# Kernel optimization log

Hardware: AMD Instinct MI355X
Metric: run time of the kernel (lower is better)

Reference implementation:

```python
import jax, jax.numpy as jnp
import numpy as np

D_MODEL = 1024
NUM_HEADS = 16
D_K = D_MODEL // NUM_HEADS


def setup_inputs() -> dict:
    key = jax.random.key(0)
    ks = jax.random.split(key, 12)
    B, S = 4, 2048
    scale = 1.0 / np.sqrt(D_MODEL)
    inp = {
        "query": jax.random.normal(ks[0], (B, S, D_MODEL), dtype=jnp.float32),
        "key": jax.random.normal(ks[1], (B, S, D_MODEL), dtype=jnp.float32),
        "value": jax.random.normal(ks[2], (B, S, D_MODEL), dtype=jnp.float32),
        "Wq": jax.random.normal(ks[3], (D_MODEL, D_MODEL), dtype=jnp.float32) * scale,
        "bq": jnp.zeros((D_MODEL,), dtype=jnp.float32),
        "Wk": jax.random.normal(ks[4], (D_MODEL, D_MODEL), dtype=jnp.float32) * scale,
        "bk": jnp.zeros((D_MODEL,), dtype=jnp.float32),
        "Wv": jax.random.normal(ks[5], (D_MODEL, D_MODEL), dtype=jnp.float32) * scale,
        "bv": jnp.zeros((D_MODEL,), dtype=jnp.float32),
        "Wo": jax.random.normal(ks[6], (D_MODEL, D_MODEL), dtype=jnp.float32) * scale,
        "bo": jnp.zeros((D_MODEL,), dtype=jnp.float32),
    }
    return inp


def reference(query, key, value, Wq, bq, Wk, bk, Wv, bv, Wo, bo):
    B, S, _ = query.shape
    # project and split heads: [B, S, D] -> [B, H, S, d_k]
    def split_heads(x):
        return x.reshape(B, -1, NUM_HEADS, D_K).transpose(0, 2, 1, 3)

    q = split_heads(query @ Wq + bq)
    k = split_heads(key @ Wk + bk)
    v = split_heads(value @ Wv + bv)

    # scores: [B, H, Sq, Sk]
    scores = jnp.einsum("bhqd,bhkd->bhqk", q, k) / jnp.sqrt(jnp.float32(D_K))
    p_attn = jax.nn.softmax(scores, axis=-1)
    out = jnp.einsum("bhqk,bhkd->bhqd", p_attn, v)  # [B, H, Sq, d_k]

    out = out.transpose(0, 2, 1, 3).reshape(B, -1, NUM_HEADS * D_K)
    return out @ Wo + bo
```

## Files before the change

kernel.cpp:

```cpp
#include <hip/hip_runtime.h>
#include <hip/hip_bf16.h>

#define D_MODEL 1024
#define SEQ     2048
#define BATCH   4
#define HEADS   16
#define DKK     64
#define MTOT    (BATCH*SEQ)

typedef __attribute__((ext_vector_type(8)))  __bf16 bf16x8;
typedef __attribute__((ext_vector_type(4)))  float  f32x4;
typedef __attribute__((ext_vector_type(16))) float  f32x16;
typedef unsigned short u16;
typedef __attribute__((address_space(1))) const unsigned GU;
typedef __attribute__((address_space(3))) unsigned LU;

__device__ __forceinline__ u16 f2bf(float f) {
    unsigned u = __builtin_bit_cast(unsigned, f);
    u += 0x7FFFu + ((u >> 16) & 1u);
    return (u16)(u >> 16);
}

__device__ __forceinline__ unsigned pk2(float a, float b) {
    u16 x = __builtin_bit_cast(u16, (__bf16)a);
    u16 y = __builtin_bit_cast(u16, (__bf16)b);
    return (unsigned)x | ((unsigned)y << 16);
}

__device__ __forceinline__ float exp2_hw(float x) {
    return __builtin_amdgcn_exp2f(x);
}

__global__ void f2b3_kernel(const float* __restrict__ q, const float* __restrict__ k,
                            const float* __restrict__ v,
                            u16* __restrict__ oq, u16* __restrict__ ok, u16* __restrict__ ov,
                            int n4) {
    const float* in = (blockIdx.y == 0) ? q : (blockIdx.y == 1) ? k : v;
    u16* out = (blockIdx.y == 0) ? oq : (blockIdx.y == 1) ? ok : ov;
    int stride = gridDim.x * blockDim.x;
    for (int i = blockIdx.x * blockDim.x + threadIdx.x; i < n4; i += stride) {
        float4 x = reinterpret_cast<const float4*>(in)[i];
        ushort4 o;
        o.x = f2bf(x.x); o.y = f2bf(x.y); o.z = f2bf(x.z); o.w = f2bf(x.w);
        reinterpret_cast<ushort4*>(out)[i] = o;
    }
}

__global__ void wtrans4_kernel(const float* __restrict__ W0, const float* __restrict__ W1,
                               const float* __restrict__ W2, const float* __restrict__ W3,
                               u16* __restrict__ T0, u16* __restrict__ T1,
                               u16* __restrict__ T2, u16* __restrict__ T3) {
    const float* W = (blockIdx.z == 0) ? W0 : (blockIdx.z == 1) ? W1 : (blockIdx.z == 2) ? W2 : W3;
    u16* Wt = (blockIdx.z == 0) ? T0 : (blockIdx.z == 1) ? T1 : (blockIdx.z == 2) ? T2 : T3;
    __shared__ float t[32][33];
    int bx = blockIdx.x * 32, by = blockIdx.y * 32;
    int x = threadIdx.x, y0 = threadIdx.y;
    for (int y = y0; y < 32; y += 8)
        t[y][x] = W[(size_t)(by + y) * D_MODEL + bx + x];
    __syncthreads();
    for (int y = y0; y < 32; y += 8)
        Wt[(size_t)(bx + y) * D_MODEL + by + x] = f2bf(t[x][y]);
}

__global__ __launch_bounds__(256) void gemm_pipe(
        const u16* __restrict__ A0, const u16* __restrict__ A1, const u16* __restrict__ A2,
        const u16* __restrict__ B0, const u16* __restrict__ B1, const u16* __restrict__ B2,
        const float* __restrict__ bi0, const float* __restrict__ bi1, const float* __restrict__ bi2,
        u16* __restrict__ o0, u16* __restrict__ o1, u16* __restrict__ o2,
        float* __restrict__ outf, int mode, float scale0)
{
    __shared__ __align__(16) char smem[3][16384];

    const int lin = blockIdx.x;
    const int xcd = lin & 7, slot = lin >> 3;
    const int cpx = gridDim.x >> 3;
    const int work = xcd * cpx + slot;
    const int xb = work & 7;
    const int yz = work >> 3;
    const int z = yz >> 6, yb = yz & 63;
    const int m0 = yb * 128, n0 = xb * 128;

    const u16* A  = (z == 0) ? A0 : (z == 1) ? A1 : A2;
    const u16* Bt = (z == 0) ? B0 : (z == 1) ? B1 : B2;
    const float* bias = (z == 0) ? bi0 : (z == 1) ? bi1 : bi2;
    u16* outb = (z == 0) ? o0 : (z == 1) ? o1 : o2;
    const float scale = (z == 0) ? scale0 : 1.0f;

    const int tid = threadIdx.x;
    const int w = tid >> 6, lane = tid & 63;
    const int l15 = lane & 15, lg = lane >> 4;
    const int wr = w >> 1, wc = w & 1;

    f32x4 acc[4][4];
#pragma unroll
    for (int i = 0; i < 4; i++)
#pragma unroll
        for (int j = 0; j < 4; j++) acc[i][j] = (f32x4){0.f, 0.f, 0.f, 0.f};

    auto stage = [&](int buf, int k0) {
        u16* Al = (u16*)(smem[buf]);
        u16* Bl = (u16*)(smem[buf] + 8192);
#pragma unroll
        for (int c = tid; c < 512; c += 256) {
            int row = c >> 2, ch = c & 3;
            __builtin_amdgcn_global_load_lds(
                (GU*)(A + (size_t)(m0 + row) * D_MODEL + k0 + ch * 8),
                (LU*)(Al + c * 8), 16, 0, 0);
            __builtin_amdgcn_global_load_lds(
                (GU*)(Bt + (size_t)(n0 + row) * D_MODEL + k0 + ch * 8),
                (LU*)(Bl + c * 8), 16, 0, 0);
        }
    };

    auto compute = [&](int buf) {
        const u16* Al = (const u16*)(smem[buf]);
        const u16* Bl = (const u16*)(smem[buf] + 8192);
        bf16x8 af[4], bfr[4];
#pragma unroll
        for (int m = 0; m < 4; m++)
            af[m] = *reinterpret_cast<const bf16x8*>(&Al[(wr * 64 + m * 16 + l15) * 32 + lg * 8]);
#pragma unroll
        for (int n = 0; n < 4; n++)
            bfr[n] = *reinterpret_cast<const bf16x8*>(&Bl[(wc * 64 + n * 16 + l15) * 32 + lg * 8]);
        __builtin_amdgcn_s_setprio(1);
#pragma unroll
        for (int m = 0; m < 4; m++)
#pragma unroll
            for (int n = 0; n < 4; n++)
                acc[m][n] = __builtin_amdgcn_mfma_f32_16x16x32_bf16(af[m], bfr[n], acc[m][n], 0, 0, 0);
        __builtin_amdgcn_s_setprio(0);
    };

    stage(0, 0);
    stage(1, 32);
    for (int t = 0; t < 32; ++t) {
        if (t < 31) asm volatile("s_waitcnt vmcnt(4)" ::: "memory");
        else        asm volatile("s_waitcnt vmcnt(0)" ::: "memory");
        __builtin_amdgcn_s_barrier();
        __builtin_amdgcn_sched_barrier(0);
        if (t + 2 < 32) stage((t + 2) % 3, (t + 2) * 32);
        compute(t % 3);
    }

    if (mode == 0 && z == 2) {
        __syncthreads();
        typedef u16 TRow[136];
        TRow* T = reinterpret_cast<TRow*>(smem);
#pragma unroll
        for (int n = 0; n < 4; n++) {
            int colL = wc * 64 + n * 16 + l15;
            float bv = bias[n0 + colL];
#pragma unroll
            for (int m = 0; m < 4; m++) {
                int rowL = wr * 64 + m * 16 + lg * 4;
#pragma unroll
                for (int r = 0; r < 4; r++)
                    T[colL][rowL + r] = f2bf(acc[m][n][r] + bv);
            }
        }
        __syncthreads();
        {
            int col = tid >> 1, half = tid & 1;
            int colG = n0 + col;
            int h = colG >> 6, d = colG & 63;
            int b = m0 >> 11, s0r = (m0 & (SEQ - 1)) + half * 64;
            u16* dst = outb + (((size_t)b * HEADS + h) * DKK + d) * SEQ + s0r;
            const u16* src = &T[col][half * 64];
#pragma unroll
            for (int c = 0; c < 8; c++)
                *reinterpret_cast<bf16x8*>(dst + c * 8) =
                    *reinterpret_cast<const bf16x8*>(src + c * 8);
        }
        return;
    }
#pragma unroll
    for (int n = 0; n < 4; n++) {
        int col = n0 + wc * 64 + n * 16 + l15;
        float bv = bias[col];
        int h = col >> 6, d = col & 63;
#pragma unroll
        for (int m = 0; m < 4; m++) {
            int rowb = m0 + wr * 64 + m * 16 + lg * 4;
            if (mode == 0) {
                int b = rowb >> 11, s0r = rowb & (SEQ - 1);
#pragma unroll
                for (int r = 0; r < 4; r++)
                    outb[(((size_t)b * HEADS + h) * SEQ + s0r + r) * DKK + d] =
                        f2bf((acc[m][n][r] + bv) * scale);
            } else {
#pragma unroll
                for (int r = 0; r < 4; r++)
                    outf[(size_t)(rowb + r) * D_MODEL + col] = acc[m][n][r] + bv;
            }
        }
    }
}

__global__ __launch_bounds__(512, 2) void attn9_kernel(
        const u16* __restrict__ Qh, const u16* __restrict__ Kh,
        const u16* __restrict__ VT, u16* __restrict__ ctx)
{
    __shared__ __align__(16) char smem[3][16384];

    const int i = blockIdx.x;
    const int xcd = i & 7, j = i >> 3;
    const int bh = xcd + 8 * (j & 7);
    const int bx = j >> 3;
    const int b = bh >> 4, h = bh & 15;
    const int tid = threadIdx.x, w = tid >> 6, lane = tid & 63;
    const int l31 = lane & 31, hi = lane >> 5;
    const int q0 = bx * 256 + w * 32;

    const u16* Qp = Qh + ((size_t)bh * SEQ + q0 + l31) * DKK + 8 * hi;
    bf16x8 qf[4];
#pragma unroll
    for (int c = 0; c < 4; c++)
        qf[c] = *reinterpret_cast<const bf16x8*>(Qp + 16 * c);

    const char* Kbyte = (const char*)(Kh + (size_t)bh * SEQ * DKK);
    const char* Vbyte = (const char*)(VT + (size_t)bh * DKK * SEQ);

    f32x16 zv;
#pragma unroll
    for (int z = 0; z < 16; z++) zv[z] = 0.f;
    f32x16 oacc0 = zv, oacc1 = zv;
    float lsum = 0.f;

    const int kr = tid >> 3, kc = tid & 7;
    const int ksw = (kc ^ (kr & 7)) * 16;
    const int krp = (kr & 51) | ((kr & 4) << 1) | ((kr & 8) >> 1);

    auto stage = [&](int buf, int kt) {
        char* Kb = smem[buf];
        char* Vb = smem[buf] + 8192;
        __builtin_amdgcn_global_load_lds((GU*)(Kbyte + (size_t)(kt + krp) * 128 + ksw),
                                         (LU*)(Kb + tid * 16), 16, 0, 0);
        __builtin_amdgcn_global_load_lds((GU*)(Vbyte + (size_t)kr * (SEQ * 2) + kt * 2 + ksw),
                                         (LU*)(Vb + tid * 16), 16, 0, 0);
    };

    auto compute = [&](int buf) {
        const char* Kb = smem[buf];
        const char* Vb = smem[buf] + 8192;
        const int xr = (l31 & 7);

        bf16x8 kf[8];
#pragma unroll
        for (int c = 0; c < 4; c++) {
            int sl = ((2 * c + hi) ^ xr) * 16;
            kf[c]     = *reinterpret_cast<const bf16x8*>(Kb + l31 * 128 + sl);
            kf[c + 4] = *reinterpret_cast<const bf16x8*>(Kb + (l31 + 32) * 128 + sl);
        }

        __builtin_amdgcn_s_setprio(1);
        f32x16 s0 = __builtin_amdgcn_mfma_f32_32x32x16_bf16(kf[0], qf[0], zv, 0, 0, 0);
        f32x16 s1 = __builtin_amdgcn_mfma_f32_32x32x16_bf16(kf[4], qf[0], zv, 0, 0, 0);
#pragma unroll
        for (int c = 1; c < 4; c++) {
            s0 = __builtin_amdgcn_mfma_f32_32x32x16_bf16(kf[c],     qf[c], s0, 0, 0, 0);
            s1 = __builtin_amdgcn_mfma_f32_32x32x16_bf16(kf[c + 4], qf[c], s1, 0, 0, 0);
        }
        __builtin_amdgcn_s_setprio(0);

#pragma unroll
        for (int i2 = 0; i2 < 16; i2++) { s0[i2] = exp2_hw(s0[i2]); s1[i2] = exp2_hw(s1[i2]); }
        float a0 = (s0[0] + s0[1]) + (s0[2] + s0[3]);
        float a1 = (s0[4] + s0[5]) + (s0[6] + s0[7]);
        float a2 = (s0[8] + s0[9]) + (s0[10] + s0[11]);
        float a3 = (s0[12] + s0[13]) + (s0[14] + s0[15]);
        float b0 = (s1[0] + s1[1]) + (s1[2] + s1[3]);
        float b1 = (s1[4] + s1[5]) + (s1[6] + s1[7]);
        float b2 = (s1[8] + s1[9]) + (s1[10] + s1[11]);
        float b3 = (s1[12] + s1[13]) + (s1[14] + s1[15]);
        lsum += ((a0 + a1) + (a2 + a3)) + ((b0 + b1) + (b2 + b3));

#pragma unroll
        for (int t = 0; t < 4; t++) {
            const int o = 8 * (t & 1);
            union { unsigned u[4]; bf16x8 v; } pu;
            if (t < 2) {
                pu.u[0] = pk2(s0[o+0], s0[o+1]);
                pu.u[1] = pk2(s0[o+2], s0[o+3]);
                pu.u[2] = pk2(s0[o+4], s0[o+5]);
                pu.u[3] = pk2(s0[o+6], s0[o+7]);
            } else {
                pu.u[0] = pk2(s1[o+0], s1[o+1]);
                pu.u[1] = pk2(s1[o+2], s1[o+3]);
                pu.u[2] = pk2(s1[o+4], s1[o+5]);
                pu.u[3] = pk2(s1[o+6], s1[o+7]);
            }
            bf16x8 pf = pu.v;

            int sl = ((2 * t + hi) ^ xr) * 16;
            bf16x8 vf0 = *reinterpret_cast<const bf16x8*>(Vb + l31 * 128 + sl);
            bf16x8 vf1 = *reinterpret_cast<const bf16x8*>(Vb + (l31 + 32) * 128 + sl);
            __builtin_amdgcn_s_setprio(1);
            oacc0 = __builtin_amdgcn_mfma_f32_32x32x16_bf16(vf0, pf, oacc0, 0, 0, 0);
            oacc1 = __builtin_amdgcn_mfma_f32_32x32x16_bf16(vf1, pf, oacc1, 0, 0, 0);
            __builtin_amdgcn_s_setprio(0);
        }
    };

    stage(0, 0);
    stage(1, 64);
    for (int t = 0; t < 32; ++t) {
        if (t < 31) asm volatile("s_waitcnt vmcnt(2)" ::: "memory");
        else        asm volatile("s_waitcnt vmcnt(0)" ::: "memory");
        __builtin_amdgcn_s_barrier();
        __builtin_amdgcn_sched_barrier(0);
        if (t + 2 < 32) stage((t + 2) % 3, (t + 2) * 64);
        compute(t % 3);
    }
    __syncthreads();

    lsum += __shfl_xor(lsum, 32, 64);
    float inv = 1.0f / lsum;

    typedef u16 OtArr[32][72];
    OtArr* Ot = reinterpret_cast<OtArr*>(smem);
#pragma unroll
    for (int r = 0; r < 16; r++) {
        int d0 = (r & 3) + 8 * (r >> 2) + 4 * hi;
        Ot[w][l31][d0]      = f2bf(oacc0[r] * inv);
        Ot[w][l31][d0 + 32] = f2bf(oacc1[r] * inv);
    }
    __syncthreads();
#pragma unroll
    for (int it = 0; it < 4; it++) {
        int r = (lane >> 3) + 8 * it, ch = lane & 7;
        bf16x8 v = *reinterpret_cast<const bf16x8*>(&Ot[w][r][ch * 8]);
        *reinterpret_cast<bf16x8*>(ctx + ((size_t)b * SEQ + q0 + r) * D_MODEL + h * DKK + ch * 8) = v;
    }
}

extern "C" void kernel_launch(void* const* d_in, const int* in_sizes, int n_in,
                              void* d_out, int out_size, void* d_ws, size_t ws_size,
                              hipStream_t stream)
{
    (void)in_sizes; (void)n_in; (void)out_size; (void)ws_size;

    const float* query = (const float*)d_in[0];
    const float* key   = (const float*)d_in[1];
    const float* value = (const float*)d_in[2];
    const float* Wq    = (const float*)d_in[3];
    const float* bq    = (const float*)d_in[4];
    const float* Wk    = (const float*)d_in[5];
    const float* bk    = (const float*)d_in[6];
    const float* Wv    = (const float*)d_in[7];
    const float* bv    = (const float*)d_in[8];
    const float* Wo    = (const float*)d_in[9];
    const float* bo    = (const float*)d_in[10];
    float* out = (float*)d_out;

    char* ws = (char*)d_ws;
    const size_t MB = 1024ull * 1024ull;
    u16* Xq  = (u16*)(ws);
    u16* Xk  = (u16*)(ws + 16 * MB);
    u16* Xv  = (u16*)(ws + 32 * MB);
    u16* Wtq = (u16*)(ws + 48 * MB);
    u16* Wtk = (u16*)(ws + 50 * MB);
    u16* Wtv = (u16*)(ws + 52 * MB);
    u16* Wto = (u16*)(ws + 54 * MB);
    u16* Qhp = (u16*)(ws + 56 * MB);
    u16* Khp = (u16*)(ws + 72 * MB);
    u16* VT  = (u16*)(ws + 88 * MB);
    u16* ctx = (u16*)(ws + 104 * MB);

    int nX4 = MTOT * D_MODEL / 4;
    f2b3_kernel<<<dim3(1024, 3), 256, 0, stream>>>(query, key, value, Xq, Xk, Xv, nX4);

    dim3 wg(32, 32, 4), wb(32, 8);
    wtrans4_kernel<<<wg, wb, 0, stream>>>(Wq, Wk, Wv, Wo, Wtq, Wtk, Wtv, Wto);

    gemm_pipe<<<1536, 256, 0, stream>>>(Xq, Xk, Xv, Wtq, Wtk, Wtv, bq, bk, bv,
                                        Qhp, Khp, VT, nullptr, 0, 0.125f * 1.44269504f);

    attn9_kernel<<<512, 512, 0, stream>>>(Qhp, Khp, VT, ctx);

    gemm_pipe<<<512, 256, 0, stream>>>(ctx, ctx, ctx, Wto, Wto, Wto, bo, bo, bo,
                                       nullptr, nullptr, nullptr, out, 1, 1.0f);
}
```

Before: 207.0 us.

## Fuse fp32-to-bf16 activation conversion into QKV projection GEMM loads

Removes the standalone conversion kernel for query/key/value and has the QKV GEMM load fp32 activations directly, convert them to bf16 in registers, and write them to LDS, while weights still use direct global-to-LDS loads. This removes a full read/write pass over the activations and one kernel launch. In exchange, the GEMM reads twice the bytes for A per tile and adds register conversion and LDS writes inside the pipelined loop, which may reduce overlap. The output GEMM is split into its own specialized kernel.

Result: no change. 203.1 us (median of 2 runs) (-1.8%).

```diff
diff --git a/kernel.cpp b/kernel.cpp
--- a/kernel.cpp
+++ b/kernel.cpp
@@ -29,21 +29,6 @@
 
 __device__ __forceinline__ float exp2_hw(float x) {
     return __builtin_amdgcn_exp2f(x);
-}
-
-__global__ void f2b3_kernel(const float* __restrict__ q, const float* __restrict__ k,
-                            const float* __restrict__ v,
-                            u16* __restrict__ oq, u16* __restrict__ ok, u16* __restrict__ ov,
-                            int n4) {
-    const float* in = (blockIdx.y == 0) ? q : (blockIdx.y == 1) ? k : v;
-    u16* out = (blockIdx.y == 0) ? oq : (blockIdx.y == 1) ? ok : ov;
-    int stride = gridDim.x * blockDim.x;
-    for (int i = blockIdx.x * blockDim.x + threadIdx.x; i < n4; i += stride) {
-        float4 x = reinterpret_cast<const float4*>(in)[i];
-        ushort4 o;
-        o.x = f2bf(x.x); o.y = f2bf(x.y); o.z = f2bf(x.z); o.w = f2bf(x.w);
-        reinterpret_cast<ushort4*>(out)[i] = o;
-    }
 }
 
 __global__ void wtrans4_kernel(const float* __restrict__ W0, const float* __restrict__ W1,
@@ -62,12 +47,11 @@
         Wt[(size_t)(bx + y) * D_MODEL + by + x] = f2bf(t[x][y]);
 }
 
-__global__ __launch_bounds__(256) void gemm_pipe(
-        const u16* __restrict__ A0, const u16* __restrict__ A1, const u16* __restrict__ A2,
+__global__ __launch_bounds__(256) void gemm_qkv(
+        const float* __restrict__ A0, const float* __restrict__ A1, const float* __restrict__ A2,
         const u16* __restrict__ B0, const u16* __restrict__ B1, const u16* __restrict__ B2,
         const float* __restrict__ bi0, const float* __restrict__ bi1, const float* __restrict__ bi2,
-        u16* __restrict__ o0, u16* __restrict__ o1, u16* __restrict__ o2,
-        float* __restrict__ outf, int mode, float scale0)
+        u16* __restrict__ o0, u16* __restrict__ o1, u16* __restrict__ o2, float qscale)
 {
     __shared__ __align__(16) char smem[3][16384];
 
@@ -80,11 +64,147 @@
     const int z = yz >> 6, yb = yz & 63;
     const int m0 = yb * 128, n0 = xb * 128;
 
-    const u16* A  = (z == 0) ? A0 : (z == 1) ? A1 : A2;
+    const float* A = (z == 0) ? A0 : (z == 1) ? A1 : A2;
     const u16* Bt = (z == 0) ? B0 : (z == 1) ? B1 : B2;
     const float* bias = (z == 0) ? bi0 : (z == 1) ? bi1 : bi2;
     u16* outb = (z == 0) ? o0 : (z == 1) ? o1 : o2;
-    const float scale = (z == 0) ? scale0 : 1.0f;
+    const float scale = (z == 0) ? qscale : 1.0f;
+
+    const int tid = threadIdx.x;
+    const int w = tid >> 6, lane = tid & 63;
+    const int l15 = lane & 15, lg = lane >> 4;
+    const int wr = w >> 1, wc = w & 1;
+
+    f32x4 acc[4][4];
+#pragma unroll
+    for (int i = 0; i < 4; i++)
+#pragma unroll
+        for (int j = 0; j < 4; j++) acc[i][j] = (f32x4){0.f, 0.f, 0.f, 0.f};
+
+    const float* Ab = A + (size_t)(m0 + (tid >> 2)) * D_MODEL + (tid & 3) * 8;
+    float4 aw, ax, ay, az_;
+
+    auto loadA = [&](int k0) {
+        const float* p0 = Ab + k0;
+        const float* p1 = p0 + (size_t)64 * D_MODEL;
+        aw  = *reinterpret_cast<const float4*>(p0);
+        ax  = *reinterpret_cast<const float4*>(p0 + 4);
+        ay  = *reinterpret_cast<const float4*>(p1);
+        az_ = *reinterpret_cast<const float4*>(p1 + 4);
+    };
+    auto cvtWriteA = [&](int buf) {
+        u16* Al = (u16*)(smem[buf]);
+        union { u16 e[8]; bf16x8 v; } u0, u1;
+        u0.e[0] = f2bf(aw.x); u0.e[1] = f2bf(aw.y); u0.e[2] = f2bf(aw.z); u0.e[3] = f2bf(aw.w);
+        u0.e[4] = f2bf(ax.x); u0.e[5] = f2bf(ax.y); u0.e[6] = f2bf(ax.z); u0.e[7] = f2bf(ax.w);
+        u1.e[0] = f2bf(ay.x); u1.e[1] = f2bf(ay.y); u1.e[2] = f2bf(ay.z); u1.e[3] = f2bf(ay.w);
+        u1.e[4] = f2bf(az_.x); u1.e[5] = f2bf(az_.y); u1.e[6] = f2bf(az_.z); u1.e[7] = f2bf(az_.w);
+        *reinterpret_cast<bf16x8*>(Al + tid * 8) = u0.v;
+        *reinterpret_cast<bf16x8*>(Al + (tid + 256) * 8) = u1.v;
+    };
+    auto gldsB = [&](int buf, int k0) {
+        u16* Bl = (u16*)(smem[buf] + 8192);
+        __builtin_amdgcn_global_load_lds(
+            (GU*)(Bt + (size_t)(n0 + (tid >> 2)) * D_MODEL + k0 + (tid & 3) * 8),
+            (LU*)(Bl + tid * 8), 16, 0, 0);
+        __builtin_amdgcn_global_load_lds(
+            (GU*)(Bt + (size_t)(n0 + (tid >> 2) + 64) * D_MODEL + k0 + (tid & 3) * 8),
+            (LU*)(Bl + (tid + 256) * 8), 16, 0, 0);
+    };
+
+    auto compute = [&](int buf) {
+        const u16* Al = (const u16*)(smem[buf]);
+        const u16* Bl = (const u16*)(smem[buf] + 8192);
+        bf16x8 af[4], bfr[4];
+#pragma unroll
+        for (int m = 0; m < 4; m++)
+            af[m] = *reinterpret_cast<const bf16x8*>(&Al[(wr * 64 + m * 16 + l15) * 32 + lg * 8]);
+#pragma unroll
+        for (int n = 0; n < 4; n++)
+            bfr[n] = *reinterpret_cast<const bf16x8*>(&Bl[(wc * 64 + n * 16 + l15) * 32 + lg * 8]);
+        __builtin_amdgcn_s_setprio(1);
+#pragma unroll
+        for (int m = 0; m < 4; m++)
+#pragma unroll
+            for (int n = 0; n < 4; n++)
+                acc[m][n] = __builtin_amdgcn_mfma_f32_16x16x32_bf16(af[m], bfr[n], acc[m][n], 0, 0, 0);
+        __builtin_amdgcn_s_setprio(0);
+    };
+
+    loadA(0);  gldsB(0, 0);
+    cvtWriteA(0);
+    loadA(32); gldsB(1, 32);
+    for (int t = 0; t < 32; ++t) {
+        if (t < 31) asm volatile("s_waitcnt vmcnt(6)" ::: "memory");
+        else        asm volatile("s_waitcnt vmcnt(0)" ::: "memory");
+        asm volatile("s_waitcnt lgkmcnt(0)" ::: "memory");
+        __builtin_amdgcn_s_barrier();
+        __builtin_amdgcn_sched_barrier(0);
+        if (t < 31) cvtWriteA((t + 1) % 3);
+        if (t + 2 < 32) { loadA((t + 2) * 32); gldsB((t + 2) % 3, (t + 2) * 32); }
+        compute(t % 3);
+    }
+
+    if (z == 2) {
+        __syncthreads();
+        typedef u16 TRow[136];
+        TRow* T = reinterpret_cast<TRow*>(smem);
+#pragma unroll
+        for (int n = 0; n < 4; n++) {
+            int colL = wc * 64 + n * 16 + l15;
+            float bv = bias[n0 + colL];
+#pragma unroll
+            for (int m = 0; m < 4; m++) {
+                int rowL = wr * 64 + m * 16 + lg * 4;
+#pragma unroll
+                for (int r = 0; r < 4; r++)
+                    T[colL][rowL + r] = f2bf(acc[m][n][r] + bv);
+            }
+        }
+        __syncthreads();
+        {
+            int col = tid >> 1, half = tid & 1;
+            int colG = n0 + col;
+            int h = colG >> 6, d = colG & 63;
+            int b = m0 >> 11, s0r = (m0 & (SEQ - 1)) + half * 64;
+            u16* dst = outb + (((size_t)b * HEADS + h) * DKK + d) * SEQ + s0r;
+            const u16* src = &T[col][half * 64];
+#pragma unroll
+            for (int c = 0; c < 8; c++)
+                *reinterpret_cast<bf16x8*>(dst + c * 8) =
+                    *reinterpret_cast<const bf16x8*>(src + c * 8);
+        }
+        return;
+    }
+#pragma unroll
+    for (int n = 0; n < 4; n++) {
+        int col = n0 + wc * 64 + n * 16 + l15;
+        float bv = bias[col];
+        int h = col >> 6, d = col & 63;
+#pragma unroll
+        for (int m = 0; m < 4; m++) {
+            int rowb = m0 + wr * 64 + m * 16 + lg * 4;
+            int b = rowb >> 11, s0r = rowb & (SEQ - 1);
+#pragma unroll
+            for (int r = 0; r < 4; r++)
+                outb[(((size_t)b * HEADS + h) * SEQ + s0r + r) * DKK + d] =
+                    f2bf((acc[m][n][r] + bv) * scale);
+        }
+    }
+}
+
+__global__ __launch_bounds__(256) void gemm_out(
+        const u16* __restrict__ A, const u16* __restrict__ Bt,
+        const float* __restrict__ bias, float* __restrict__ outf)
+{
+    __shared__ __align__(16) char smem[3][16384];
+
+    const int lin = blockIdx.x;
+    const int xcd = lin & 7, slot = lin >> 3;
+    const int cpx = gridDim.x >> 3;
+    const int work = xcd * cpx + slot;
+    const int xb = work & 7, yb = work >> 3;
+    const int m0 = yb * 128, n0 = xb * 128;
 
     const int tid = threadIdx.x;
     const int w = tid >> 6, lane = tid & 63;
@@ -111,7 +231,6 @@
                 (LU*)(Bl + c * 8), 16, 0, 0);
         }
     };
-
     auto compute = [&](int buf) {
         const u16* Al = (const u16*)(smem[buf]);
         const u16* Bl = (const u16*)(smem[buf] + 8192);
@@ -142,56 +261,16 @@
         compute(t % 3);
     }
 
-    if (mode == 0 && z == 2) {
-        __syncthreads();
-        typedef u16 TRow[136];
-        TRow* T = reinterpret_cast<TRow*>(smem);
-#pragma unroll
-        for (int n = 0; n < 4; n++) {
-            int colL = wc * 64 + n * 16 + l15;
-            float bv = bias[n0 + colL];
-#pragma unroll
-            for (int m = 0; m < 4; m++) {
-                int rowL = wr * 64 + m * 16 + lg * 4;
-#pragma unroll
-                for (int r = 0; r < 4; r++)
-                    T[colL][rowL + r] = f2bf(acc[m][n][r] + bv);
-            }
-        }
-        __syncthreads();
-        {
-            int col = tid >> 1, half = tid & 1;
-            int colG = n0 + col;
-            int h = colG >> 6, d = colG & 63;
-            int b = m0 >> 11, s0r = (m0 & (SEQ - 1)) + half * 64;
-            u16* dst = outb + (((size_t)b * HEADS + h) * DKK + d) * SEQ + s0r;
-            const u16* src = &T[col][half * 64];
-#pragma unroll
-            for (int c = 0; c < 8; c++)
-                *reinterpret_cast<bf16x8*>(dst + c * 8) =
-                    *reinterpret_cast<const bf16x8*>(src + c * 8);
-        }
-        return;
-    }
 #pragma unroll
     for (int n = 0; n < 4; n++) {
         int col = n0 + wc * 64 + n * 16 + l15;
         float bv = bias[col];
-        int h = col >> 6, d = col & 63;
 #pragma unroll
         for (int m = 0; m < 4; m++) {
             int rowb = m0 + wr * 64 + m * 16 + lg * 4;
-            if (mode == 0) {
-                int b = rowb >> 11, s0r = rowb & (SEQ - 1);
-#pragma unroll
-                for (int r = 0; r < 4; r++)
-                    outb[(((size_t)b * HEADS + h) * SEQ + s0r + r) * DKK + d] =
-                        f2bf((acc[m][n][r] + bv) * scale);
-            } else {
-#pragma unroll
-                for (int r = 0; r < 4; r++)
-                    outf[(size_t)(rowb + r) * D_MODEL + col] = acc[m][n][r] + bv;
-            }
+#pragma unroll
+            for (int r = 0; r < 4; r++)
+                outf[(size_t)(rowb + r) * D_MODEL + col] = acc[m][n][r] + bv;
         }
     }
 }
@@ -354,9 +433,6 @@
 
     char* ws = (char*)d_ws;
     const size_t MB = 1024ull * 1024ull;
-    u16* Xq  = (u16*)(ws);
-    u16* Xk  = (u16*)(ws + 16 * MB);
-    u16* Xv  = (u16*)(ws + 32 * MB);
     u16* Wtq = (u16*)(ws + 48 * MB);
     u16* Wtk = (u16*)(ws + 50 * MB);
     u16* Wtv = (u16*)(ws + 52 * MB);
@@ -366,17 +442,13 @@
     u16* VT  = (u16*)(ws + 88 * MB);
     u16* ctx = (u16*)(ws + 104 * MB);
 
-    int nX4 = MTOT * D_MODEL / 4;
-    f2b3_kernel<<<dim3(1024, 3), 256, 0, stream>>>(query, key, value, Xq, Xk, Xv, nX4);
-
     dim3 wg(32, 32, 4), wb(32, 8);
     wtrans4_kernel<<<wg, wb, 0, stream>>>(Wq, Wk, Wv, Wo, Wtq, Wtk, Wtv, Wto);
 
-    gemm_pipe<<<1536, 256, 0, stream>>>(Xq, Xk, Xv, Wtq, Wtk, Wtv, bq, bk, bv,
-                                        Qhp, Khp, VT, nullptr, 0, 0.125f * 1.44269504f);
+    gemm_qkv<<<1536, 256, 0, stream>>>(query, key, value, Wtq, Wtk, Wtv, bq, bk, bv,
+                                       Qhp, Khp, VT, 0.125f * 1.44269504f);
 
     attn9_kernel<<<512, 512, 0, stream>>>(Qhp, Khp, VT, ctx);
 
-    gemm_pipe<<<512, 256, 0, stream>>>(ctx, ctx, ctx, Wto, Wto, Wto, bo, bo, bo,
-                                       nullptr, nullptr, nullptr, out, 1, 1.0f);
-}
+    gemm_out<<<512, 256, 0, stream>>>(ctx, Wto, bo, out);
+}
```
